# Kernel optimization log

Hardware: AMD Instinct MI355X
Metric: run time of the kernel (lower is better)

## Reference

```python
import jax, jax.numpy as jnp
import numpy as np

B, N, DIN, DOUT, S, ITERS = 32, 2048, 512, 512, 2, 3
HID = max(DOUT, 128)  # mlp hidden = max(dim_out, hidden_dim)
EPS = 1e-8
LN_EPS = 1e-5  # torch LayerNorm default
SCALE = DOUT ** -0.5


def layernorm(x, g, b):
    m = jnp.mean(x, axis=-1, keepdims=True)
    v = jnp.mean(jnp.square(x - m), axis=-1, keepdims=True)
    return (x - m) * jax.lax.rsqrt(v + LN_EPS) * g + b


def setup_inputs() -> dict:
    key = jax.random.key(0)
    ks = jax.random.split(key, 16)
    w = lambda k, shp: jax.random.normal(k, shp, dtype=jnp.float32) * 0.02
    return {
        "inputs": jax.random.normal(ks[0], (B, N, DIN), dtype=jnp.float32),
        "shared_init_slots": jax.random.normal(ks[1], (B, S, DOUT), dtype=jnp.float32),
        "Wq": w(ks[2], (DOUT, DOUT)), "bq": jnp.zeros((DOUT,), jnp.float32),
        "Wk": w(ks[3], (DIN, DOUT)), "bk": jnp.zeros((DOUT,), jnp.float32),
        "Wv": w(ks[4], (DIN, DOUT)), "bv": jnp.zeros((DOUT,), jnp.float32),
        "ln_in_g": jnp.ones((DIN,), jnp.float32), "ln_in_b": jnp.zeros((DIN,), jnp.float32),
        "ln_s_g": jnp.ones((DOUT,), jnp.float32), "ln_s_b": jnp.zeros((DOUT,), jnp.float32),
        "ln_f_g": jnp.ones((DOUT,), jnp.float32), "ln_f_b": jnp.zeros((DOUT,), jnp.float32),
        "gru_wih": w(ks[5], (3 * DOUT, DOUT)), "gru_whh": w(ks[6], (3 * DOUT, DOUT)),
        "gru_bih": jnp.zeros((3 * DOUT,), jnp.float32), "gru_bhh": jnp.zeros((3 * DOUT,), jnp.float32),
        "W1": w(ks[7], (DOUT, HID)), "b1": jnp.zeros((HID,), jnp.float32),
        "W2": w(ks[8], (HID, DOUT)), "b2": jnp.zeros((DOUT,), jnp.float32),
    }


def reference(inputs, shared_init_slots, Wq, bq, Wk, bk, Wv, bv,
              ln_in_g, ln_in_b, ln_s_g, ln_s_b, ln_f_g, ln_f_b,
              gru_wih, gru_whh, gru_bih, gru_bhh, W1, b1, W2, b2):
    x = layernorm(inputs, ln_in_g, ln_in_b)          # [B,N,DIN]
    k = x @ Wk + bk                                   # [B,N,DOUT]
    v = x @ Wv + bv                                   # [B,N,DOUT]
    slots = shared_init_slots                         # [B,S,DOUT]
    for _ in range(ITERS):
        slots_prev = slots
        s = layernorm(slots, ln_s_g, ln_s_b)
        q = s @ Wq + bq                               # [B,S,DOUT]
        dots = jnp.einsum('bid,bjd->bij', q, k) * SCALE   # [B,S,N]
        attn_pre = jax.nn.softmax(dots, axis=1)       # softmax over SLOT dim (custom)
        attn = attn_pre / (jnp.sum(attn_pre, axis=-1, keepdims=True) + EPS)
        updates = jnp.einsum('bjd,bij->bid', v, attn)  # [B,S,DOUT]
        # GRUCell: h' = (1-z)*n + z*h, gate order r,z,n (torch convention)
        u = updates.reshape(-1, DOUT)
        h = slots_prev.reshape(-1, DOUT)
        gx = u @ gru_wih.T + gru_bih                  # [B*S, 3*DOUT]
        gh = h @ gru_whh.T + gru_bhh
        xr, xz, xn = jnp.split(gx, 3, axis=-1)
        hr, hz, hn = jnp.split(gh, 3, axis=-1)
        r = jax.nn.sigmoid(xr + hr)
        z = jax.nn.sigmoid(xz + hz)
        n_gate = jnp.tanh(xn + r * hn)
        h_new = (1.0 - z) * n_gate + z * h
        # residual MLP
        hln = layernorm(h_new, ln_f_g, ln_f_b)
        h_new = h_new + (jax.nn.relu(hln @ W1 + b1) @ W2 + b2)
        slots = h_new.reshape(B, S, DOUT)
    return slots, q, k, attn
```

## Files before the change

### kernel.cpp

```cpp
#include <hip/hip_runtime.h>
#include <stdint.h>

typedef __bf16 bf16_t;
typedef bf16_t bf16x8 __attribute__((ext_vector_type(8)));
typedef float f32x4 __attribute__((ext_vector_type(4)));

typedef unsigned int u32;
typedef __attribute__((address_space(1))) const u32 gu32;
typedef __attribute__((address_space(3))) u32 lu32;

#define LN_EPS 1e-5f
#define EPS_ 1e-8f
#define SCALE_ 0.04419417382415922f

__device__ __forceinline__ float wave_red_sum(float v) {
#pragma unroll
  for (int off = 32; off > 0; off >>= 1) v += __shfl_xor(v, off, 64);
  return v;
}

__global__ __launch_bounds__(256) void transpose_prep(
    const float* __restrict__ Wk, const float* __restrict__ Wv,
    const float* __restrict__ wih, const float* __restrict__ whh,
    bf16_t* __restrict__ BT, float* __restrict__ wihT, float* __restrict__ whhT)
{
  int z = blockIdx.z;
  if (z < 2 && blockIdx.y >= 16) return;
  const float* src = (z == 0) ? Wk : (z == 1) ? Wv : (z == 2) ? wih : whh;
  __shared__ float tile[32][33];
  int tx = threadIdx.x & 31, ty = threadIdx.x >> 5;
  int row0 = blockIdx.y * 32, col0 = blockIdx.x * 32;
#pragma unroll
  for (int i = 0; i < 4; ++i)
    tile[ty + 8 * i][tx] = src[(size_t)(row0 + ty + 8 * i) * 512 + col0 + tx];
  __syncthreads();
  if (z < 2) {
#pragma unroll
    for (int i = 0; i < 4; ++i)
      BT[(size_t)(z * 512 + col0 + ty + 8 * i) * 512 + row0 + tx] =
          (bf16_t)tile[tx][ty + 8 * i];
  } else {
    float* dst = (z == 2) ? wihT : whhT;
#pragma unroll
    for (int i = 0; i < 4; ++i)
      dst[(size_t)(col0 + ty + 8 * i) * 1536 + row0 + tx] = tile[tx][ty + 8 * i];
  }
}

__global__ __launch_bounds__(256) void small_prep(
    const float* __restrict__ bk, const float* __restrict__ bv,
    const float* __restrict__ slots_init,
    float* __restrict__ biasc, float* __restrict__ slots)
{
  int idx = blockIdx.x * 256 + threadIdx.x;
  if (idx < 1024) {
    biasc[idx] = (idx < 512) ? bk[idx] : bv[idx - 512];
  } else {
    int i = idx - 1024;
    slots[i] = slots_init[i];
  }
}

__global__ __launch_bounds__(256) void ln_apply(
    const float* __restrict__ in, const float* __restrict__ lng,
    const float* __restrict__ lnb, bf16_t* __restrict__ xbf)
{
  int w = threadIdx.x >> 6, lane = threadIdx.x & 63;
  size_t row = (size_t)blockIdx.x * 4 + w;
  const float4* rp = (const float4*)(in + row * 512);
  float4 a = rp[lane * 2], c = rp[lane * 2 + 1];
  float s1 = a.x + a.y + a.z + a.w + c.x + c.y + c.z + c.w;
  float s2 = a.x * a.x + a.y * a.y + a.z * a.z + a.w * a.w +
             c.x * c.x + c.y * c.y + c.z * c.z + c.w * c.w;
  s1 = wave_red_sum(s1);
  s2 = wave_red_sum(s2);
  float mean = s1 * (1.f / 512.f);
  float var = s2 * (1.f / 512.f) - mean * mean;
  float rs = rsqrtf(var + LN_EPS);
  float4 g0 = *(const float4*)&lng[lane * 8];
  float4 g1 = *(const float4*)&lng[lane * 8 + 4];
  float4 b0 = *(const float4*)&lnb[lane * 8];
  float4 b1 = *(const float4*)&lnb[lane * 8 + 4];
  bf16x8 o;
  o[0] = (bf16_t)((a.x - mean) * rs * g0.x + b0.x);
  o[1] = (bf16_t)((a.y - mean) * rs * g0.y + b0.y);
  o[2] = (bf16_t)((a.z - mean) * rs * g0.z + b0.z);
  o[3] = (bf16_t)((a.w - mean) * rs * g0.w + b0.w);
  o[4] = (bf16_t)((c.x - mean) * rs * g1.x + b1.x);
  o[5] = (bf16_t)((c.y - mean) * rs * g1.y + b1.y);
  o[6] = (bf16_t)((c.z - mean) * rs * g1.z + b1.z);
  o[7] = (bf16_t)((c.w - mean) * rs * g1.w + b1.w);
  *(bf16x8*)&xbf[row * 512 + lane * 8] = o;
}

__global__ __launch_bounds__(256) void gemm_kv(
    const bf16_t* __restrict__ xbf, const bf16_t* __restrict__ BT,
    const float* __restrict__ biasc,
    float* __restrict__ out_k, bf16_t* __restrict__ vbf, bf16_t* kbf)
{
  __shared__ __align__(16) char smem[32768];

  const int tid = threadIdx.x, lane = tid & 63, w = tid >> 6;
  const int quad = lane >> 4, l16 = lane & 15;
  const int l = blockIdx.x;
  const int x = l & 7, t0 = l >> 3;
  const int n0 = (t0 & 7) * 128;
  const int m0 = ((t0 >> 3) * 8 + x) * 128;
  const int mb = (w & 1) * 64, nb = (w >> 1) * 64;
  const int swz = (l16 >> 1) & 3;

  const bf16_t* a_base = xbf + (size_t)m0 * 512;
  const bf16_t* b_base = BT + (size_t)n0 * 512;

  f32x4 acc[4][4] = {};

  auto stage = [&](int buf, int kk) {
    bf16_t* As = (bf16_t*)(smem + buf * 16384);
    bf16_t* Bs = (bf16_t*)(smem + buf * 16384 + 8192);
#pragma unroll
    for (int r = 0; r < 2; ++r) {
      int tt = tid + r * 256;
      int rr = tt >> 2, pg = tt & 3;
      int lg = pg ^ ((rr >> 1) & 3);
      __builtin_amdgcn_global_load_lds((gu32*)(a_base + (size_t)rr * 512 + kk + lg * 8),
                                       (lu32*)&As[tt * 8], 16, 0, 0);
      __builtin_amdgcn_global_load_lds((gu32*)(b_base + (size_t)rr * 512 + kk + lg * 8),
                                       (lu32*)&Bs[tt * 8], 16, 0, 0);
    }
  };

  auto compute = [&](int buf) {
    const bf16_t* As = (const bf16_t*)(smem + buf * 16384);
    const bf16_t* Bs = (const bf16_t*)(smem + buf * 16384 + 8192);
    bf16x8 af[4], bfr[4];
#pragma unroll
    for (int mt = 0; mt < 4; ++mt)
      af[mt] = *(const bf16x8*)&As[(mb + mt * 16 + l16) * 32 + ((quad ^ swz) * 8)];
#pragma unroll
    for (int nt = 0; nt < 4; ++nt)
      bfr[nt] = *(const bf16x8*)&Bs[(nb + nt * 16 + l16) * 32 + ((quad ^ swz) * 8)];
#pragma unroll
    for (int mt = 0; mt < 4; ++mt)
#pragma unroll
      for (int nt = 0; nt < 4; ++nt)
        acc[mt][nt] = __builtin_amdgcn_mfma_f32_16x16x32_bf16(af[mt], bfr[nt], acc[mt][nt], 0, 0, 0);
  };

  stage(0, 0);
  __syncthreads();
#pragma unroll
  for (int t = 0; t < 16; ++t) {
    if (t < 15) stage((t + 1) & 1, (t + 1) * 32);
    compute(t & 1);
    if (t < 15) __syncthreads();
  }

  const int is_k = (n0 < 512);
  const int rbase = m0 + mb + quad * 4;
  if (is_k) {
#pragma unroll
    for (int nt = 0; nt < 4; ++nt) {
      int col = n0 + nb + nt * 16 + l16;
      float bias = biasc[col];
#pragma unroll
      for (int mt = 0; mt < 4; ++mt) {
        int row = rbase + mt * 16;
#pragma unroll
        for (int r = 0; r < 4; ++r) {
          float v = acc[mt][nt][r] + bias;
          out_k[(size_t)(row + r) * 512 + col] = v;
        }
      }
    }
    if (kbf) {
#pragma unroll
      for (int nt = 0; nt < 4; ++nt) {
        int col = n0 + nb + nt * 16 + l16;
        float bias = biasc[col];
#pragma unroll
        for (int mt = 0; mt < 4; ++mt) {
          int row = rbase + mt * 16;
#pragma unroll
          for (int r = 0; r < 4; ++r)
            kbf[(size_t)(row + r) * 512 + col] = (bf16_t)(acc[mt][nt][r] + bias);
        }
      }
    }
  } else {
#pragma unroll
    for (int nt = 0; nt < 4; ++nt) {
      int colg = n0 + nb + nt * 16 + l16;
      float bias = biasc[colg];
      int col = colg - 512;
#pragma unroll
      for (int mt = 0; mt < 4; ++mt) {
        int row = rbase + mt * 16;
#pragma unroll
        for (int r = 0; r < 4; ++r)
          vbf[(size_t)(row + r) * 512 + col] = (bf16_t)(acc[mt][nt][r] + bias);
      }
    }
  }
}

__global__ __launch_bounds__(256) void ln_q_kernel(
    const float* __restrict__ slots,
    const float* __restrict__ lnsg, const float* __restrict__ lnsb,
    const float* __restrict__ Wq, const float* __restrict__ bq,
    float* __restrict__ q_out)
{
  __shared__ float s[2][512];
  __shared__ float part[4][2][64];
  __shared__ float red1[4], red2[4];
  int tid = threadIdx.x, w = tid >> 6, lane = tid & 63;
  int b = blockIdx.x >> 3, cg = blockIdx.x & 7;

  int r = tid >> 7;
  int off = (tid * 4) & 511;
  float4 v = *(const float4*)&slots[b * 1024 + tid * 4];
  float s1 = v.x + v.y + v.z + v.w;
  float s2 = v.x * v.x + v.y * v.y + v.z * v.z + v.w * v.w;
  s1 = wave_red_sum(s1);
  s2 = wave_red_sum(s2);
  if (lane == 0) { red1[w] = s1; red2[w] = s2; }
  __syncthreads();
  float mean = (red1[r * 2] + red1[r * 2 + 1]) * (1.f / 512.f);
  float var = (red2[r * 2] + red2[r * 2 + 1]) * (1.f / 512.f) - mean * mean;
  float rstd = rsqrtf(var + LN_EPS);
  float4 g4 = *(const float4*)&lnsg[off];
  float4 b4 = *(const float4*)&lnsb[off];
  s[r][off + 0] = (v.x - mean) * rstd * g4.x + b4.x;
  s[r][off + 1] = (v.y - mean) * rstd * g4.y + b4.y;
  s[r][off + 2] = (v.z - mean) * rstd * g4.z + b4.z;
  s[r][off + 3] = (v.w - mean) * rstd * g4.w + b4.w;
  __syncthreads();

  int c = cg * 64 + lane;
  float a0 = 0.f, a1 = 0.f;
  for (int d = w * 128; d < w * 128 + 128; ++d) {
    float wv = Wq[d * 512 + c];
    a0 += s[0][d] * wv;
    a1 += s[1][d] * wv;
  }
  part[w][0][lane] = a0;
  part[w][1][lane] = a1;
  __syncthreads();
  if (tid < 128) {
    int rr = tid >> 6, ll = tid & 63;
    float sum = part[0][rr][ll] + part[1][rr][ll] + part[2][rr][ll] + part[3][rr][ll]
              + bq[cg * 64 + ll];
    q_out[(b * 2 + rr) * 512 + cg * 64 + ll] = sum;
  }
}

__global__ __launch_bounds__(256) void attend_fused(
    const float* __restrict__ kf, const bf16_t* __restrict__ vbf,
    const float* __restrict__ qf,
    float* __restrict__ upd_part, float* __restrict__ rs_part,
    float* __restrict__ attn_pre)
{
  __shared__ float qs[2][528];
  __shared__ float p_s[2][64];
  int tid = threadIdx.x, w = tid >> 6, lane = tid & 63;
  int b = blockIdx.x >> 5, chunk = blockIdx.x & 31;
  int j0 = chunk * 64;

  {
    int slot = tid >> 7, pos = (tid & 127) * 4;
    int dq = pos >> 7, dd = pos & 127;
    *(f32x4*)&qs[slot][dq * 132 + dd] = *(const f32x4*)&qf[b * 1024 + slot * 512 + pos];
  }
  __syncthreads();

  int jj = lane & 15;
  int dq = lane >> 4;
  const float* kp = kf + (size_t)(b * 2048 + j0 + w * 16 + jj) * 512 + dq * 128;
  const float* qb0 = &qs[0][dq * 132];
  const float* qb1 = &qs[1][dq * 132];
  float dot0 = 0.f, dot1 = 0.f;
#pragma unroll
  for (int h = 0; h < 4; ++h) {
    f32x4 kr[8];
#pragma unroll
    for (int i = 0; i < 8; ++i) kr[i] = *(const f32x4*)(kp + h * 32 + i * 4);
#pragma unroll
    for (int i = 0; i < 8; ++i) {
      f32x4 qa = *(const f32x4*)(qb0 + h * 32 + i * 4);
      f32x4 qc = *(const f32x4*)(qb1 + h * 32 + i * 4);
#pragma unroll
      for (int t = 0; t < 4; ++t) {
        dot0 += kr[i][t] * qa[t];
        dot1 += kr[i][t] * qc[t];
      }
    }
  }
  dot0 += __shfl_xor(dot0, 16, 64);
  dot0 += __shfl_xor(dot0, 32, 64);
  dot1 += __shfl_xor(dot1, 16, 64);
  dot1 += __shfl_xor(dot1, 32, 64);
  float d0f = dot0 * SCALE_, d1f = dot1 * SCALE_;
  float mx = fmaxf(d0f, d1f);
  float e0 = __expf(d0f - mx), e1 = __expf(d1f - mx);
  float inv = 1.f / (e0 + e1);
  float p0 = e0 * inv, p1 = e1 * inv;
  if (lane < 16) {
    int jj2 = w * 16 + lane;
    p_s[0][jj2] = p0;
    p_s[1][jj2] = p1;
    attn_pre[(b * 2 + 0) * 2048 + j0 + jj2] = p0;
    attn_pre[(b * 2 + 1) * 2048 + j0 + jj2] = p1;
  }
  __syncthreads();

  if (w == 0) {
    float a = p_s[0][lane];
    float c = p_s[1][lane];
    a = wave_red_sum(a);
    c = wave_red_sum(c);
    if (lane == 0) {
      rs_part[(b * 2 + 0) * 32 + chunk] = a;
      rs_part[(b * 2 + 1) * 32 + chunk] = c;
    }
  }

  float u0[8] = {}, u1[8] = {};
  const bf16_t* vp = vbf + (size_t)(b * 2048 + j0 + w * 16) * 512 + lane * 8;
  for (int t = 0; t < 16; ++t) {
    float p0b = p_s[0][w * 16 + t];
    float p1b = p_s[1][w * 16 + t];
    bf16x8 vv = *(const bf16x8*)(vp + (size_t)t * 512);
#pragma unroll
    for (int tt = 0; tt < 8; ++tt) {
      float vfl = (float)vv[tt];
      u0[tt] += p0b * vfl;
      u1[tt] += p1b * vfl;
    }
  }
  float* up0 = upd_part + ((size_t)(chunk * 4 + w) * 64 + b * 2 + 0) * 512 + lane * 8;
  f32x4 w0a = {u0[0], u0[1], u0[2], u0[3]}, w0b = {u0[4], u0[5], u0[6], u0[7]};
  f32x4 w1a = {u1[0], u1[1], u1[2], u1[3]}, w1b = {u1[4], u1[5], u1[6], u1[7]};
  *(f32x4*)(up0) = w0a;
  *(f32x4*)(up0 + 4) = w0b;
  *(f32x4*)(up0 + 512) = w1a;
  *(f32x4*)(up0 + 516) = w1b;
}

__global__ __launch_bounds__(256) void attend_bf16(
    const bf16_t* __restrict__ kbf, const bf16_t* __restrict__ vbf,
    const float* __restrict__ qf,
    float* __restrict__ upd_part, float* __restrict__ rs_part,
    float* __restrict__ attn_pre)
{
  __shared__ float qs[2][528];
  __shared__ float p_s[2][64];
  int tid = threadIdx.x, w = tid >> 6, lane = tid & 63;
  int b = blockIdx.x >> 5, chunk = blockIdx.x & 31;
  int j0 = chunk * 64;

  {
    int slot = tid >> 7, pos = (tid & 127) * 4;
    int dq = pos >> 7, dd = pos & 127;
    *(f32x4*)&qs[slot][dq * 132 + dd] = *(const f32x4*)&qf[b * 1024 + slot * 512 + pos];
  }
  __syncthreads();

  int jj = lane & 15;
  int dq = lane >> 4;
  const bf16_t* kp = kbf + (size_t)(b * 2048 + j0 + w * 16 + jj) * 512 + dq * 128;
  const float* qb0 = &qs[0][dq * 132];
  const float* qb1 = &qs[1][dq * 132];
  float dot0 = 0.f, dot1 = 0.f;
#pragma unroll
  for (int h = 0; h < 2; ++h) {
    bf16x8 kr[8];
#pragma unroll
    for (int i = 0; i < 8; ++i) kr[i] = *(const bf16x8*)(kp + h * 64 + i * 8);
#pragma unroll
    for (int i = 0; i < 8; ++i) {
      f32x4 qa0 = *(const f32x4*)(qb0 + h * 64 + i * 8);
      f32x4 qa1 = *(const f32x4*)(qb0 + h * 64 + i * 8 + 4);
      f32x4 qc0 = *(const f32x4*)(qb1 + h * 64 + i * 8);
      f32x4 qc1 = *(const f32x4*)(qb1 + h * 64 + i * 8 + 4);
#pragma unroll
      for (int t = 0; t < 4; ++t) {
        float klo = (float)kr[i][t], khi = (float)kr[i][t + 4];
        dot0 += klo * qa0[t] + khi * qa1[t];
        dot1 += klo * qc0[t] + khi * qc1[t];
      }
    }
  }
  dot0 += __shfl_xor(dot0, 16, 64);
  dot0 += __shfl_xor(dot0, 32, 64);
  dot1 += __shfl_xor(dot1, 16, 64);
  dot1 += __shfl_xor(dot1, 32, 64);
  float d0f = dot0 * SCALE_, d1f = dot1 * SCALE_;
  float mx = fmaxf(d0f, d1f);
  float e0 = __expf(d0f - mx), e1 = __expf(d1f - mx);
  float inv = 1.f / (e0 + e1);
  float p0 = e0 * inv, p1 = e1 * inv;
  if (lane < 16) {
    int jj2 = w * 16 + lane;
    p_s[0][jj2] = p0;
    p_s[1][jj2] = p1;
    attn_pre[(b * 2 + 0) * 2048 + j0 + jj2] = p0;
    attn_pre[(b * 2 + 1) * 2048 + j0 + jj2] = p1;
  }
  __syncthreads();

  if (w == 0) {
    float a = p_s[0][lane];
    float c = p_s[1][lane];
    a = wave_red_sum(a);
    c = wave_red_sum(c);
    if (lane == 0) {
      rs_part[(b * 2 + 0) * 32 + chunk] = a;
      rs_part[(b * 2 + 1) * 32 + chunk] = c;
    }
  }

  float u0[8] = {}, u1[8] = {};
  const bf16_t* vp = vbf + (size_t)(b * 2048 + j0 + w * 16) * 512 + lane * 8;
  for (int t = 0; t < 16; ++t) {
    float p0b = p_s[0][w * 16 + t];
    float p1b = p_s[1][w * 16 + t];
    bf16x8 vv = *(const bf16x8*)(vp + (size_t)t * 512);
#pragma unroll
    for (int tt = 0; tt < 8; ++tt) {
      float vfl = (float)vv[tt];
      u0[tt] += p0b * vfl;
      u1[tt] += p1b * vfl;
    }
  }
  float* up0 = upd_part + ((size_t)(chunk * 4 + w) * 64 + b * 2 + 0) * 512 + lane * 8;
  f32x4 w0a = {u0[0], u0[1], u0[2], u0[3]}, w0b = {u0[4], u0[5], u0[6], u0[7]};
  f32x4 w1a = {u1[0], u1[1], u1[2], u1[3]}, w1b = {u1[4], u1[5], u1[6], u1[7]};
  *(f32x4*)(up0) = w0a;
  *(f32x4*)(up0 + 4) = w0b;
  *(f32x4*)(up0 + 512) = w1a;
  *(f32x4*)(up0 + 516) = w1b;
}

__global__ __launch_bounds__(512) void reduce_upd(
    const float* __restrict__ upd_part, const float* __restrict__ rs_part,
    float* __restrict__ upd, float* __restrict__ rowsum)
{
  int r = blockIdx.x, tid = threadIdx.x;
  const float* p = upd_part + (size_t)r * 512 + tid;
  float acc = 0.f;
#pragma unroll 8
  for (int i = 0; i < 128; ++i) acc += p[(size_t)i * 32768];
  upd[r * 512 + tid] = acc;
  if (tid < 64) {
    float v = (tid < 32) ? rs_part[r * 32 + tid] : 0.f;
    v = wave_red_sum(v);
    if (tid == 0) rowsum[r] = v;
  }
}

__global__ __launch_bounds__(256) void gates_kernel(
    const float* __restrict__ slots, const float* __restrict__ upd,
    const float* __restrict__ rowsum,
    const float* __restrict__ wihT, const float* __restrict__ whhT,
    const float* __restrict__ bih, const float* __restrict__ bhh,
    float* __restrict__ gx, float* __restrict__ gh)
{
  __shared__ float in_s[2][512];
  __shared__ float part[4][2][256];
  int tid = threadIdx.x, w = tid >> 6, lane = tid & 63;
  int rg = blockIdx.x / 12, cc = blockIdx.x % 12;
  int is_gh = (cc >= 6);
  int ccl = is_gh ? cc - 6 : cc;
  {
    int rr = tid >> 7, pos = (tid & 127) * 4;
    int row = rg * 2 + rr;
    const float* src = (is_gh ? slots : upd) + row * 512;
    f32x4 v = *(const f32x4*)&src[pos];
    if (!is_gh) v *= 1.f / (rowsum[row] + EPS_);
    *(f32x4*)&in_s[rr][pos] = v;
  }
  __syncthreads();
  int c0 = ccl * 256 + lane * 4;
  const float* __restrict__ W = is_gh ? whhT : wihT;
  f32x4 acc0 = {0.f, 0.f, 0.f, 0.f}, acc1 = acc0;
  for (int d = w * 128; d < w * 128 + 128; ++d) {
    f32x4 w4 = *(const f32x4*)&W[d * 1536 + c0];
    acc0 += in_s[0][d] * w4;
    acc1 += in_s[1][d] * w4;
  }
  *(f32x4*)&part[w][0][lane * 4] = acc0;
  *(f32x4*)&part[w][1][lane * 4] = acc1;
  __syncthreads();
  if (tid < 128) {
    int r = tid >> 6, ll = tid & 63;
    int cf = ccl * 256 + ll * 4;
    f32x4 s = *(const f32x4*)&part[0][r][ll * 4];
    s += *(const f32x4*)&part[1][r][ll * 4];
    s += *(const f32x4*)&part[2][r][ll * 4];
    s += *(const f32x4*)&part[3][r][ll * 4];
    s += *(const f32x4*)&(is_gh ? bhh : bih)[cf];
    *(f32x4*)&(is_gh ? gh : gx)[(rg * 2 + r) * 1536 + cf] = s;
  }
}

__global__ __launch_bounds__(512) void gru_ln_kernel(
    const float* __restrict__ gx, const float* __restrict__ gh,
    const float* __restrict__ slots,
    const float* __restrict__ lnf_g, const float* __restrict__ lnf_b,
    float* __restrict__ hnew, float* __restrict__ hln)
{
  __shared__ float red1[8], red2[8];
  int tid = threadIdx.x, row = blockIdx.x;
  float gxr = gx[row * 1536 + tid], gxz = gx[row * 1536 + 512 + tid], gxn = gx[row * 1536 + 1024 + tid];
  float ghr = gh[row * 1536 + tid], ghz = gh[row * 1536 + 512 + tid], ghn = gh[row * 1536 + 1024 + tid];
  float h = slots[row * 512 + tid];
  float r_ = 1.f / (1.f + __expf(-(gxr + ghr)));
  float z_ = 1.f / (1.f + __expf(-(gxz + ghz)));
  float n_ = tanhf(gxn + r_ * ghn);
  float hn = (1.f - z_) * n_ + z_ * h;
  hnew[row * 512 + tid] = hn;
  float s1 = wave_red_sum(hn), s2 = wave_red_sum(hn * hn);
  int w = tid >> 6, lane = tid & 63;
  if (lane == 0) { red1[w] = s1; red2[w] = s2; }
  __syncthreads();
  s1 = 0.f; s2 = 0.f;
#pragma unroll
  for (int i = 0; i < 8; ++i) { s1 += red1[i]; s2 += red2[i]; }
  float mean = s1 * (1.f / 512.f);
  float var = s2 * (1.f / 512.f) - mean * mean;
  float rstd = rsqrtf(var + LN_EPS);
  hln[row * 512 + tid] = (hn - mean) * rstd * lnf_g[tid] + lnf_b[tid];
}

__global__ __launch_bounds__(256) void mlp1_kernel(
    const float* __restrict__ hln, const float* __restrict__ W1,
    const float* __restrict__ b1, float* __restrict__ act)
{
  __shared__ float in_s[2][512];
  __shared__ float part[4][2][64];
  int tid = threadIdx.x, w = tid >> 6, lane = tid & 63;
  int rg = blockIdx.x >> 3, cc = blockIdx.x & 7;
  {
    int rr = tid >> 7, pos = (tid & 127) * 4;
    *(f32x4*)&in_s[rr][pos] = *(const f32x4*)&hln[(rg * 2 + rr) * 512 + pos];
  }
  __syncthreads();
  int c = cc * 64 + lane;
  float a0 = 0.f, a1 = 0.f;
  for (int d = w * 128; d < w * 128 + 128; ++d) {
    float wv = W1[d * 512 + c];
    a0 += in_s[0][d] * wv;
    a1 += in_s[1][d] * wv;
  }
  part[w][0][lane] = a0;
  part[w][1][lane] = a1;
  __syncthreads();
  if (tid < 128) {
    int r = tid >> 6, ll = tid & 63;
    float s = part[0][r][ll] + part[1][r][ll] + part[2][r][ll] + part[3][r][ll]
            + b1[cc * 64 + ll];
    act[(rg * 2 + r) * 512 + cc * 64 + ll] = fmaxf(s, 0.f);
  }
}

__global__ __launch_bounds__(256) void mlp2_kernel(
    const float* __restrict__ act, const float* __restrict__ W2,
    const float* __restrict__ b2, const float* __restrict__ hnew,
    float* __restrict__ slots)
{
  __shared__ float in_s[2][512];
  __shared__ float part[4][2][64];
  int tid = threadIdx.x, w = tid >> 6, lane = tid & 63;
  int rg = blockIdx.x >> 3, cc = blockIdx.x & 7;
  {
    int rr = tid >> 7, pos = (tid & 127) * 4;
    *(f32x4*)&in_s[rr][pos] = *(const f32x4*)&act[(rg * 2 + rr) * 512 + pos];
  }
  __syncthreads();
  int c = cc * 64 + lane;
  float a0 = 0.f, a1 = 0.f;
  for (int d = w * 128; d < w * 128 + 128; ++d) {
    float wv = W2[d * 512 + c];
    a0 += in_s[0][d] * wv;
    a1 += in_s[1][d] * wv;
  }
  part[w][0][lane] = a0;
  part[w][1][lane] = a1;
  __syncthreads();
  if (tid < 128) {
    int r = tid >> 6, ll = tid & 63;
    int row = rg * 2 + r, c2 = cc * 64 + ll;
    float s = part[0][r][ll] + part[1][r][ll] + part[2][r][ll] + part[3][r][ll] + b2[c2];
    slots[row * 512 + c2] = hnew[row * 512 + c2] + s;
  }
}

__global__ __launch_bounds__(256) void norm_attn(
    const float* __restrict__ rowsum, float* __restrict__ attn)
{
  int idx = blockIdx.x * 256 + threadIdx.x;
  int row = idx >> 11;
  attn[idx] = attn[idx] / (rowsum[row] + EPS_);
}

extern "C" void kernel_launch(void* const* d_in, const int* in_sizes, int n_in,
                              void* d_out, int out_size, void* d_ws, size_t ws_size,
                              hipStream_t stream)
{
  const float* inputs     = (const float*)d_in[0];
  const float* slots_init = (const float*)d_in[1];
  const float* Wq   = (const float*)d_in[2];
  const float* bq   = (const float*)d_in[3];
  const float* Wk   = (const float*)d_in[4];
  const float* bk   = (const float*)d_in[5];
  const float* Wv   = (const float*)d_in[6];
  const float* bv   = (const float*)d_in[7];
  const float* ln_in_g = (const float*)d_in[8];
  const float* ln_in_b = (const float*)d_in[9];
  const float* ln_s_g  = (const float*)d_in[10];
  const float* ln_s_b  = (const float*)d_in[11];
  const float* ln_f_g  = (const float*)d_in[12];
  const float* ln_f_b  = (const float*)d_in[13];
  const float* wih  = (const float*)d_in[14];
  const float* whh  = (const float*)d_in[15];
  const float* bih  = (const float*)d_in[16];
  const float* bhh  = (const float*)d_in[17];
  const float* W1   = (const float*)d_in[18];
  const float* b1   = (const float*)d_in[19];
  const float* W2   = (const float*)d_in[20];
  const float* b2   = (const float*)d_in[21];

  float* out   = (float*)d_out;
  float* slots = out;
  float* q_out = out + 32768;
  float* k_out = out + 65536;
  float* attnp = out + 33619968;

  char* ws = (char*)d_ws;
  bf16_t* xbf   = (bf16_t*)(ws);
  float*  upd_part = (float*)(ws);
  float*  rs_part  = (float*)(ws + 16777216);
  bf16_t* vbf   = (bf16_t*)(ws + 67108864);
  bf16_t* BT    = (bf16_t*)(ws + 134217728);
  float*  gx    = (float*)(ws + 134217728);
  float*  gh    = (float*)(ws + 134610944);
  float*  hnew  = (float*)(ws + 135004160);
  float*  hln   = (float*)(ws + 135135232);
  float*  wihT  = (float*)(ws + 135266304);
  float*  whhT  = (float*)(ws + 138412032);
  float*  biasc = (float*)(ws + 141557760);
  float*  act   = (float*)(ws + 141561856);
  float*  upd   = (float*)(ws + 142086144);
  float*  rowsum= (float*)(ws + 142217216);

  const size_t kbf_off = 142217472ull;
  const bool big_ws = ws_size >= kbf_off + 67108864ull;
  bf16_t* kbf = big_ws ? (bf16_t*)(ws + kbf_off) : (bf16_t*)nullptr;

  transpose_prep<<<dim3(16, 48, 4), 256, 0, stream>>>(Wk, Wv, wih, whh, BT, wihT, whhT);
  small_prep<<<132, 256, 0, stream>>>(bk, bv, slots_init, biasc, slots);
  ln_apply<<<16384, 256, 0, stream>>>(inputs, ln_in_g, ln_in_b, xbf);
  gemm_kv<<<4096, 256, 0, stream>>>(xbf, BT, biasc, k_out, vbf, kbf);
  for (int it = 0; it < 3; ++it) {
    ln_q_kernel<<<256, 256, 0, stream>>>(slots, ln_s_g, ln_s_b, Wq, bq, q_out);
    if (big_ws)
      attend_bf16<<<1024, 256, 0, stream>>>(kbf, vbf, q_out, upd_part, rs_part, attnp);
    else
      attend_fused<<<1024, 256, 0, stream>>>(k_out, vbf, q_out, upd_part, rs_part, attnp);
    reduce_upd<<<64, 512, 0, stream>>>(upd_part, rs_part, upd, rowsum);
    gates_kernel<<<384, 256, 0, stream>>>(slots, upd, rowsum, wihT, whhT, bih, bhh, gx, gh);
    gru_ln_kernel<<<64, 512, 0, stream>>>(gx, gh, slots, ln_f_g, ln_f_b, hnew, hln);
    mlp1_kernel<<<256, 256, 0, stream>>>(hln, W1, b1, act);
    mlp2_kernel<<<256, 256, 0, stream>>>(act, W2, b2, hnew, slots);
  }
  norm_attn<<<512, 256, 0, stream>>>(rowsum, attnp);
}
```

Baseline: 617.6 us.

## Restructure attend q·k dot to coalesced row loads with LDS cross-lane reduction

Each lane now reads a contiguous 8-element slice of every key row, so the wave loads whole 1 KB rows coalesced, and q is held in registers instead of staged through shared memory. Per-lane partial dots are written to a padded LDS buffer and reduced by lane pairs, followed by the two-slot softmax. This removes the strided 128-element-per-lane key access and the per-iteration shared q loads. It costs a larger shared buffer (about 35 KB), extra LDS traffic and an extra barrier.

```diff
diff --git a/kernel.cpp b/kernel.cpp
--- a/kernel.cpp
+++ b/kernel.cpp
@@ -351,59 +351,51 @@
     float* __restrict__ upd_part, float* __restrict__ rs_part,
     float* __restrict__ attn_pre)
 {
-  __shared__ float qs[2][528];
+  __shared__ float red[2][64][68];
   __shared__ float p_s[2][64];
   int tid = threadIdx.x, w = tid >> 6, lane = tid & 63;
   int b = blockIdx.x >> 5, chunk = blockIdx.x & 31;
   int j0 = chunk * 64;
 
-  {
-    int slot = tid >> 7, pos = (tid & 127) * 4;
-    int dq = pos >> 7, dd = pos & 127;
-    *(f32x4*)&qs[slot][dq * 132 + dd] = *(const f32x4*)&qf[b * 1024 + slot * 512 + pos];
-  }
-  __syncthreads();
-
-  int jj = lane & 15;
-  int dq = lane >> 4;
-  const bf16_t* kp = kbf + (size_t)(b * 2048 + j0 + w * 16 + jj) * 512 + dq * 128;
-  const float* qb0 = &qs[0][dq * 132];
-  const float* qb1 = &qs[1][dq * 132];
-  float dot0 = 0.f, dot1 = 0.f;
-#pragma unroll
-  for (int h = 0; h < 2; ++h) {
-    bf16x8 kr[8];
-#pragma unroll
-    for (int i = 0; i < 8; ++i) kr[i] = *(const bf16x8*)(kp + h * 64 + i * 8);
-#pragma unroll
-    for (int i = 0; i < 8; ++i) {
-      f32x4 qa0 = *(const f32x4*)(qb0 + h * 64 + i * 8);
-      f32x4 qa1 = *(const f32x4*)(qb0 + h * 64 + i * 8 + 4);
-      f32x4 qc0 = *(const f32x4*)(qb1 + h * 64 + i * 8);
-      f32x4 qc1 = *(const f32x4*)(qb1 + h * 64 + i * 8 + 4);
-#pragma unroll
-      for (int t = 0; t < 4; ++t) {
-        float klo = (float)kr[i][t], khi = (float)kr[i][t + 4];
-        dot0 += klo * qa0[t] + khi * qa1[t];
-        dot1 += klo * qc0[t] + khi * qc1[t];
-      }
-    }
-  }
-  dot0 += __shfl_xor(dot0, 16, 64);
-  dot0 += __shfl_xor(dot0, 32, 64);
-  dot1 += __shfl_xor(dot1, 16, 64);
-  dot1 += __shfl_xor(dot1, 32, 64);
-  float d0f = dot0 * SCALE_, d1f = dot1 * SCALE_;
-  float mx = fmaxf(d0f, d1f);
-  float e0 = __expf(d0f - mx), e1 = __expf(d1f - mx);
-  float inv = 1.f / (e0 + e1);
-  float p0 = e0 * inv, p1 = e1 * inv;
-  if (lane < 16) {
-    int jj2 = w * 16 + lane;
-    p_s[0][jj2] = p0;
-    p_s[1][jj2] = p1;
-    attn_pre[(b * 2 + 0) * 2048 + j0 + jj2] = p0;
-    attn_pre[(b * 2 + 1) * 2048 + j0 + jj2] = p1;
+  const float* qb = qf + b * 1024;
+  f32x4 q0a = *(const f32x4*)(qb + lane * 8);
+  f32x4 q0b = *(const f32x4*)(qb + lane * 8 + 4);
+  f32x4 q1a = *(const f32x4*)(qb + 512 + lane * 8);
+  f32x4 q1b = *(const f32x4*)(qb + 512 + lane * 8 + 4);
+
+  const bf16_t* kp = kbf + (size_t)(b * 2048 + j0 + w * 16) * 512 + lane * 8;
+#pragma unroll
+  for (int j = 0; j < 16; ++j) {
+    bf16x8 kk = *(const bf16x8*)(kp + (size_t)j * 512);
+    float d0 = 0.f, d1 = 0.f;
+#pragma unroll
+    for (int t = 0; t < 4; ++t) {
+      float klo = (float)kk[t], khi = (float)kk[t + 4];
+      d0 += klo * q0a[t] + khi * q0b[t];
+      d1 += klo * q1a[t] + khi * q1b[t];
+    }
+    red[0][w * 16 + j][lane] = d0;
+    red[1][w * 16 + j][lane] = d1;
+  }
+  __syncthreads();
+
+  int pr = lane >> 1, half = lane & 1;
+  int slot = pr >> 4, jl = pr & 15;
+  const float* rr = &red[slot][w * 16 + jl][half * 32];
+  f32x4 s4 = {0.f, 0.f, 0.f, 0.f};
+#pragma unroll
+  for (int k = 0; k < 8; ++k) s4 += *(const f32x4*)(rr + k * 4);
+  float s = s4[0] + s4[1] + s4[2] + s4[3];
+  s += __shfl_xor(s, 1, 64);
+  float d = s * SCALE_;
+  float dother = __shfl_xor(d, 32, 64);
+  float mx = fmaxf(d, dother);
+  float e = __expf(d - mx), eo = __expf(dother - mx);
+  float inv = 1.f / (e + eo);
+  float p = e * inv;
+  if (half == 0) {
+    p_s[slot][w * 16 + jl] = p;
+    attn_pre[(b * 2 + slot) * 2048 + j0 + w * 16 + jl] = p;
   }
   __syncthreads();
 
```

Result: faster. 598.3 us (-3.1%).
